# Optimization experiments

Measured on AMD Instinct MI355X. Metric: run time of the kernel, lower is better.

The kernel has to match this reference:

```python
import jax, jax.numpy as jnp
import numpy as np
from jax import lax

# channels holding diagonal entries of the embedded 4x4 bA (16:32) and bW (32:48)
_DIAG_CH = np.array([16, 21, 26, 31, 32, 37, 42, 47])
_EPS = 1e-4  # Tikhonov term for per-pixel matrix inversion stability


def _interp_matrix(out_n, in_n):
    """Dense 1D bicubic (a=-0.75) align_corners=True interpolation matrix, torch-compatible."""
    if out_n == in_n:
        return jnp.eye(out_n, dtype=jnp.float32)
    a = -0.75
    scale = (in_n - 1) / (out_n - 1)
    src = np.arange(out_n) * scale
    i0 = np.floor(src).astype(np.int64)
    W = np.zeros((out_n, in_n), np.float64)
    rows = np.arange(out_n)
    for k in range(-1, 3):
        t = np.abs(src - (i0 + k))
        w = np.where(t <= 1.0, (a + 2) * t**3 - (a + 3) * t**2 + 1.0,
                     np.where(t < 2.0, a * t**3 - 5 * a * t**2 + 8 * a * t - 4 * a, 0.0))
        np.add.at(W, (rows, np.clip(i0 + k, 0, in_n - 1)), w)  # border replication
    return jnp.asarray(W, jnp.float32)


def _conv(x, w, b):
    y = lax.conv_general_dilated(x, w, (1, 1), 'SAME',
                                 dimension_numbers=('NCHW', 'OIHW', 'NCHW'))
    return y + b[None, :, None, None]


def _leaky(x):
    return jnp.where(x >= 0, x, 0.01 * x)


def _mm_features(x):
    """compute_mm + intensity: x is (b,48,h,w) -> (b,17,h,w)."""
    b, c, h, w = x.shape
    v = jnp.moveaxis(x, 1, -1)                 # (b,h,w,48)
    F = v[..., :16].reshape(b, h, w, 4, 4)     # intensity frames
    A = v[..., 16:32].reshape(b, h, w, 4, 4)   # analyzer calib bA
    Wm = v[..., 32:48].reshape(b, h, w, 4, 4)  # generator calib bW
    eye = _EPS * jnp.eye(4, dtype=x.dtype)
    M = jnp.linalg.inv(A + eye) @ F @ jnp.linalg.inv(Wm + eye)  # M = A^-1 F W^-1
    inten = v[..., :16].mean(-1)[:, None]      # (b,1,h,w)
    m = jnp.moveaxis(M.reshape(b, h, w, 16), -1, 1)  # (b,16,h,w)
    return jnp.concatenate([inten, m], axis=1)


def _maxpool4(x):
    b, c, h, w = x.shape
    return x.reshape(b, c, h // 4, 4, w // 4, 4).max(axis=(3, 5))


def setup_inputs() -> dict:
    key = jax.random.key(0)
    ks = jax.random.split(key, 6)
    x = 0.3 * jax.random.normal(ks[0], (2, 48, 512, 512), jnp.float32)
    diag = jnp.asarray(_DIAG_CH)
    x = x.at[:, diag].add(1.0)  # well-conditioned per-pixel bA/bW ~ I + noise

    def bias48():
        return jnp.zeros((48,), jnp.float32).at[diag].set(1.0)

    iW0 = 0.05 * jax.random.normal(ks[1], (48, 48, 3, 3), jnp.float32)
    iW1 = 0.05 * jax.random.normal(ks[2], (48, 48, 3, 3), jnp.float32)
    oW0 = 0.05 * jax.random.normal(ks[3], (17, 17, 3, 3), jnp.float32)
    oW1 = 0.05 * jax.random.normal(ks[4], (17, 17, 3, 3), jnp.float32)
    return dict(x=x,
                iW0=iW0, iB0=bias48(), iW1=iW1, iB1=bias48(),
                oW0=oW0, oB0=jnp.zeros((17,), jnp.float32),
                oW1=oW1, oB1=jnp.zeros((17,), jnp.float32))


def reference(x, iW0, iB0, iW1, iB1, oW0, oB0, oW1, oB1):
    b, _, h, w = x.shape
    iparams = [(iW0, iB0), (iW1, iB1)]
    oparams = [(oW0, oB0), (oW1, oB1)]
    outs = []
    for lvl in range(2):  # fixed pyramid levels
        x = _leaky(_conv(x, *iparams[lvl]))
        m = _mm_features(x)                       # (b,17,hl,wl)
        Wh = _interp_matrix(h, m.shape[2])
        Ww = _interp_matrix(w, m.shape[3])
        m = jnp.einsum('Oh,bchw->bcOw', Wh, m)    # bicubic upsample rows
        m = jnp.einsum('Pw,bchw->bchP', Ww, m)    # bicubic upsample cols
        m = _leaky(_conv(m, *oparams[lvl]))
        outs.append(m)
        x = _maxpool4(x)
    return jnp.concatenate(outs, axis=1)          # (b,34,h,w)
```

## Files before the change

### kernel.cpp

```cpp
#include <hip/hip_runtime.h>
#include <math.h>


__device__ __forceinline__ float leakyf(float t) { return t >= 0.0f ? t : 0.01f * t; }

template<int CIN, int OCPT, int PX, int TW>
__global__ __launch_bounds__(256, 2)
void conv3x3_leaky(const float* __restrict__ in, const float* __restrict__ wgt,
                   const float* __restrict__ bias, float* __restrict__ out,
                   int H, int W, int COUT, int NG,
                   int in_bstride, int out_bstride, int out_coff)
{
    constexpr int XG     = TW / PX;
    constexpr int TH     = 256 / XG;
    constexpr int COLS   = TW + 2;
    constexpr int ROWS   = TH + 2;
    constexpr int STRIDE = (COLS + 3) & ~3;
    constexpr int TSZ    = ROWS * STRIDE;
    constexpr int ELEMS  = ROWS * COLS;
    constexpr int K      = (ELEMS + 255) / 256;
    constexpr int NV     = PX + 2;

    __shared__ float tile[2 * TSZ];
    __shared__ float wlds[CIN * OCPT * 12];
    __shared__ float blds[OCPT];

    const int tid   = threadIdx.x;
    const int tx    = tid & (XG - 1);
    const int ty    = tid / XG;
    const int g     = blockIdx.z % NG;
    const int b     = blockIdx.z / NG;
    const int obase = g * OCPT;
    const int row0  = blockIdx.y * TH;
    const int col0  = blockIdx.x * TW;
    const int HW    = H * W;

    for (int idx = tid; idx < CIN * OCPT * 9; idx += 256) {
        int c  = idx / (OCPT * 9);
        int r2 = idx - c * (OCPT * 9);
        int o  = r2 / 9;
        int k2 = r2 - o * 9;
        int og = obase + o;
        wlds[(c * OCPT + o) * 12 + k2] = (og < COUT) ? wgt[(og * CIN + c) * 9 + k2] : 0.0f;
    }
    if (tid < OCPT) {
        int og = obase + tid;
        blds[tid] = (og < COUT) ? bias[og] : 0.0f;
    }

    int goff[K], loff[K];
#pragma unroll
    for (int k = 0; k < K; ++k) {
        int idx = tid + k * 256;
        if (idx < ELEMS) {
            int r  = idx / COLS;
            int cc = idx - r * COLS;
            int gr = row0 - 1 + r;
            int gc = col0 - 1 + cc;
            bool v = (gr >= 0 && gr < H && gc >= 0 && gc < W);
            goff[k] = v ? (gr * W + gc) : -1;
            loff[k] = r * STRIDE + cc;
        } else {
            goff[k] = -1;
            loff[k] = -1;
        }
    }

    const float* inb = in + b * in_bstride;

    float sreg[K];
    {
        const float* ic = inb;
#pragma unroll
        for (int k = 0; k < K; ++k) {
            float v = 0.0f;
            if (goff[k] >= 0) v = ic[goff[k]];
            sreg[k] = v;
        }
#pragma unroll
        for (int k = 0; k < K; ++k)
            if (loff[k] >= 0) tile[loff[k]] = sreg[k];
    }
    __syncthreads();

    float acc[OCPT][PX];
#pragma unroll
    for (int o = 0; o < OCPT; ++o)
#pragma unroll
        for (int p = 0; p < PX; ++p) acc[o][p] = 0.0f;

    for (int c = 0; c < CIN; ++c) {
        if (c + 1 < CIN) {
            const float* ic = inb + (c + 1) * HW;
#pragma unroll
            for (int k = 0; k < K; ++k) {
                float v = 0.0f;
                if (goff[k] >= 0) v = ic[goff[k]];
                sreg[k] = v;
            }
        }

        {
            const float* tb = &tile[(c & 1) * TSZ];
            float v[3][NV];
#pragma unroll
            for (int rr = 0; rr < 3; ++rr) {
                const float* tp = tb + (ty + rr) * STRIDE + tx * PX;
                float4 a0 = *(const float4*)tp;
                v[rr][0] = a0.x; v[rr][1] = a0.y; v[rr][2] = a0.z; v[rr][3] = a0.w;
                if constexpr (PX == 8) {
                    float4 a1 = *(const float4*)(tp + 4);
                    float2 a2 = *(const float2*)(tp + 8);
                    v[rr][4] = a1.x; v[rr][5] = a1.y; v[rr][6] = a1.z; v[rr][7] = a1.w;
                    v[rr][8] = a2.x; v[rr][9] = a2.y;
                } else {
                    float2 a1 = *(const float2*)(tp + 4);
                    v[rr][4] = a1.x; v[rr][5] = a1.y;
                }
            }
#pragma unroll
            for (int o = 0; o < OCPT; ++o) {
                const float* wp = &wlds[(c * OCPT + o) * 12];
                float4 w0 = *(const float4*)wp;
                float4 w1 = *(const float4*)(wp + 4);
                float w8 = wp[8];
                float wk[9] = {w0.x, w0.y, w0.z, w0.w, w1.x, w1.y, w1.z, w1.w, w8};
#pragma unroll
                for (int px = 0; px < PX; ++px) {
                    float s = acc[o][px];
#pragma unroll
                    for (int kr = 0; kr < 3; ++kr)
#pragma unroll
                        for (int kc = 0; kc < 3; ++kc)
                            s = fmaf(wk[kr * 3 + kc], v[kr][px + kc], s);
                    acc[o][px] = s;
                }
            }
        }

        if (c + 1 < CIN) {
            float* tb = &tile[((c + 1) & 1) * TSZ];
#pragma unroll
            for (int k = 0; k < K; ++k)
                if (loff[k] >= 0) tb[loff[k]] = sreg[k];
            __syncthreads();
        }
    }

    const int orow = row0 + ty;
    float* outb = out + b * out_bstride;
#pragma unroll
    for (int o = 0; o < OCPT; ++o) {
        int og = obase + o;
        if (og < COUT) {
            float bv = blds[o];
            float r[PX];
#pragma unroll
            for (int p = 0; p < PX; ++p) { float t = acc[o][p] + bv; r[p] = leakyf(t); }
            float* op = outb + ((out_coff + og) * H + orow) * W + col0 + tx * PX;
#pragma unroll
            for (int q = 0; q < PX / 4; ++q)
                *(float4*)(op + 4 * q) = make_float4(r[4*q], r[4*q+1], r[4*q+2], r[4*q+3]);
        }
    }
}

__device__ __forceinline__ void inv4x4(const double* m, double* invOut)
{
    double inv[16];
    inv[0]  =  m[5]*m[10]*m[15] - m[5]*m[11]*m[14] - m[9]*m[6]*m[15] + m[9]*m[7]*m[14] + m[13]*m[6]*m[11] - m[13]*m[7]*m[10];
    inv[4]  = -m[4]*m[10]*m[15] + m[4]*m[11]*m[14] + m[8]*m[6]*m[15] - m[8]*m[7]*m[14] - m[12]*m[6]*m[11] + m[12]*m[7]*m[10];
    inv[8]  =  m[4]*m[9]*m[15]  - m[4]*m[11]*m[13] - m[8]*m[5]*m[15] + m[8]*m[7]*m[13] + m[12]*m[5]*m[11] - m[12]*m[7]*m[9];
    inv[12] = -m[4]*m[9]*m[14]  + m[4]*m[10]*m[13] + m[8]*m[5]*m[14] - m[8]*m[6]*m[13] - m[12]*m[5]*m[10] + m[12]*m[6]*m[9];
    inv[1]  = -m[1]*m[10]*m[15] + m[1]*m[11]*m[14] + m[9]*m[2]*m[15] - m[9]*m[3]*m[14] - m[13]*m[2]*m[11] + m[13]*m[3]*m[10];
    inv[5]  =  m[0]*m[10]*m[15] - m[0]*m[11]*m[14] - m[8]*m[2]*m[15] + m[8]*m[3]*m[14] + m[12]*m[2]*m[11] - m[12]*m[3]*m[10];
    inv[9]  = -m[0]*m[9]*m[15]  + m[0]*m[11]*m[13] + m[8]*m[1]*m[15] - m[8]*m[3]*m[13] - m[12]*m[1]*m[11] + m[12]*m[3]*m[9];
    inv[13] =  m[0]*m[9]*m[14]  - m[0]*m[10]*m[13] - m[8]*m[1]*m[14] + m[8]*m[2]*m[13] + m[12]*m[1]*m[10] - m[12]*m[2]*m[9];
    inv[2]  =  m[1]*m[6]*m[15]  - m[1]*m[7]*m[14]  - m[5]*m[2]*m[15] + m[5]*m[3]*m[14] + m[13]*m[2]*m[7]  - m[13]*m[3]*m[6];
    inv[6]  = -m[0]*m[6]*m[15]  + m[0]*m[7]*m[14]  + m[4]*m[2]*m[15] - m[4]*m[3]*m[14] - m[12]*m[2]*m[7]  + m[12]*m[3]*m[6];
    inv[10] =  m[0]*m[5]*m[15]  - m[0]*m[7]*m[13]  - m[4]*m[1]*m[15] + m[4]*m[3]*m[13] + m[12]*m[1]*m[7]  - m[12]*m[3]*m[5];
    inv[14] = -m[0]*m[5]*m[14]  + m[0]*m[6]*m[13]  + m[4]*m[1]*m[14] - m[4]*m[2]*m[13] - m[12]*m[1]*m[6]  + m[12]*m[2]*m[5];
    inv[3]  = -m[1]*m[6]*m[11]  + m[1]*m[7]*m[10]  + m[5]*m[2]*m[11] - m[5]*m[3]*m[10] - m[9]*m[2]*m[7]   + m[9]*m[3]*m[6];
    inv[7]  =  m[0]*m[6]*m[11]  - m[0]*m[7]*m[10]  - m[4]*m[2]*m[11] + m[4]*m[3]*m[10] + m[8]*m[2]*m[7]   - m[8]*m[3]*m[6];
    inv[11] = -m[0]*m[5]*m[11]  + m[0]*m[7]*m[9]   + m[4]*m[1]*m[11] - m[4]*m[3]*m[9]  - m[8]*m[1]*m[7]   + m[8]*m[3]*m[5];
    inv[15] =  m[0]*m[5]*m[10]  - m[0]*m[6]*m[9]   - m[4]*m[1]*m[10] + m[4]*m[2]*m[9]  + m[8]*m[1]*m[6]   - m[8]*m[2]*m[5];
    double det = m[0]*inv[0] + m[1]*inv[4] + m[2]*inv[8] + m[3]*inv[12];
    det = 1.0 / det;
#pragma unroll
    for (int i = 0; i < 16; ++i) invOut[i] = inv[i] * det;
}

__device__ __forceinline__ void matmul4(const double* A, const double* B, double* C)
{
#pragma unroll
    for (int r = 0; r < 4; ++r)
#pragma unroll
        for (int c = 0; c < 4; ++c) {
            double s = 0.0;
#pragma unroll
            for (int k = 0; k < 4; ++k) s += A[r * 4 + k] * B[k * 4 + c];
            C[r * 4 + c] = s;
        }
}

__global__ __launch_bounds__(256)
void mm_features_kernel(const float* __restrict__ y, float* __restrict__ m, int HW, int n)
{
    int p = blockIdx.x * 256 + threadIdx.x;
    if (p >= n) return;
    int b  = p / HW;
    int sp = p - b * HW;
    const float* base = y + (size_t)b * 48 * HW + sp;

    double A[16];
#pragma unroll
    for (int i = 0; i < 16; ++i) {
        double e = (i == 0 || i == 5 || i == 10 || i == 15) ? 1e-4 : 0.0;
        A[i] = (double)base[(16 + i) * HW] + e;
    }
    double iA[16];
    inv4x4(A, iA);

    double F[16];
    double s = 0.0;
#pragma unroll
    for (int i = 0; i < 16; ++i) { F[i] = (double)base[i * HW]; }
#pragma unroll
    for (int i = 0; i < 16; ++i) s += F[i];
    s *= (1.0 / 16.0);

    double T[16];
    matmul4(iA, F, T);

    double Wm[16];
#pragma unroll
    for (int i = 0; i < 16; ++i) {
        double e = (i == 0 || i == 5 || i == 10 || i == 15) ? 1e-4 : 0.0;
        Wm[i] = (double)base[(32 + i) * HW] + e;
    }
    double iW[16];
    inv4x4(Wm, iW);

    double M[16];
    matmul4(T, iW, M);

    float* ob = m + (size_t)b * 17 * HW + sp;
    ob[0] = (float)s;
#pragma unroll
    for (int i = 0; i < 16; ++i) ob[(1 + i) * HW] = (float)M[i];
}

__global__ __launch_bounds__(256)
void maxpool4_kernel(const float* __restrict__ in, float* __restrict__ out, int n)
{
    int idx = blockIdx.x * 256 + threadIdx.x;
    if (idx >= n) return;
    int ow = idx & 127;
    int oh = (idx >> 7) & 127;
    int ct = idx >> 14;
    const float* p = in + ct * 262144 + (oh * 4) * 512 + ow * 4;
    float mx = -3.4e38f;
#pragma unroll
    for (int r = 0; r < 4; ++r) {
        float4 v = *(const float4*)(p + r * 512);
        mx = fmaxf(mx, fmaxf(fmaxf(v.x, v.y), fmaxf(v.z, v.w)));
    }
    out[idx] = mx;
}

__device__ __forceinline__ double cubw(double t)
{
    const double a = -0.75;
    t = fabs(t);
    if (t <= 1.0) return ((a + 2.0) * t - (a + 3.0)) * t * t + 1.0;
    if (t < 2.0)  return (((t - 5.0) * t + 8.0) * t - 4.0) * a;
    return 0.0;
}

__global__ __launch_bounds__(256)
void bicubic_up4_kernel(const float* __restrict__ src, float* __restrict__ dst, int n)
{
    int idx = blockIdx.x * 256 + threadIdx.x;
    if (idx >= n) return;
    int P  = idx & 511;
    int O  = (idx >> 9) & 511;
    int bc = idx >> 18;
    const double scale = 127.0 / 511.0;
    double sh = O * scale, sw = P * scale;
    int i0 = (int)floor(sh), j0 = (int)floor(sw);
    double wh[4], ww[4];
#pragma unroll
    for (int k = 0; k < 4; ++k) {
        wh[k] = cubw(sh - (double)(i0 + k - 1));
        ww[k] = cubw(sw - (double)(j0 + k - 1));
    }
    const float* sp = src + bc * 16384;
    double acc = 0.0;
#pragma unroll
    for (int ki = 0; ki < 4; ++ki) {
        int ih = min(max(i0 - 1 + ki, 0), 127);
        double rs = 0.0;
#pragma unroll
        for (int kj = 0; kj < 4; ++kj) {
            int iw = min(max(j0 - 1 + kj, 0), 127);
            rs += ww[kj] * (double)sp[ih * 128 + iw];
        }
        acc += wh[ki] * rs;
    }
    dst[idx] = (float)acc;
}

extern "C" void kernel_launch(void* const* d_in, const int* in_sizes, int n_in,
                              void* d_out, int out_size, void* d_ws, size_t ws_size,
                              hipStream_t stream)
{
    const float* x   = (const float*)d_in[0];
    const float* iW0 = (const float*)d_in[1];
    const float* iB0 = (const float*)d_in[2];
    const float* iW1 = (const float*)d_in[3];
    const float* iB1 = (const float*)d_in[4];
    const float* oW0 = (const float*)d_in[5];
    const float* oB0 = (const float*)d_in[6];
    const float* oW1 = (const float*)d_in[7];
    const float* oB1 = (const float*)d_in[8];
    float* out = (float*)d_out;
    float* ws  = (float*)d_ws;

    float* y0 = ws;
    float* m0 = ws + 25165824;
    float* x1 = ws + 34078720;
    float* y1 = ws + 35651584;
    float* m1 = ws + 37224448;
    float* u  = ws;

    conv3x3_leaky<48, 8, 8, 64><<<dim3(8, 16, 12), 256, 0, stream>>>(
        x, iW0, iB0, y0, 512, 512, 48, 6, 48 * 512 * 512, 48 * 512 * 512, 0);
    mm_features_kernel<<<(2 * 512 * 512) / 256, 256, 0, stream>>>(y0, m0, 512 * 512, 2 * 512 * 512);
    conv3x3_leaky<17, 9, 8, 64><<<dim3(8, 16, 4), 256, 0, stream>>>(
        m0, oW0, oB0, out, 512, 512, 17, 2, 17 * 512 * 512, 34 * 512 * 512, 0);
    maxpool4_kernel<<<(2 * 48 * 128 * 128) / 256, 256, 0, stream>>>(y0, x1, 2 * 48 * 128 * 128);

    conv3x3_leaky<48, 4, 4, 32><<<dim3(4, 4, 24), 256, 0, stream>>>(
        x1, iW1, iB1, y1, 128, 128, 48, 12, 48 * 128 * 128, 48 * 128 * 128, 0);
    mm_features_kernel<<<(2 * 128 * 128) / 256, 256, 0, stream>>>(y1, m1, 128 * 128, 2 * 128 * 128);
    bicubic_up4_kernel<<<(2 * 17 * 512 * 512) / 256, 256, 0, stream>>>(m1, u, 2 * 17 * 512 * 512);
    conv3x3_leaky<17, 9, 8, 64><<<dim3(8, 16, 4), 256, 0, stream>>>(
        u, oW1, oB1, out, 512, 512, 17, 2, 17 * 512 * 512, 34 * 512 * 512, 17);
}
```

Measured before the change: 694.9 us.

## Use per-wavefront halo tiles to drop block barriers; compute bicubic in fp32

```diff
diff --git a/kernel.cpp b/kernel.cpp
--- a/kernel.cpp
+++ b/kernel.cpp
@@ -13,21 +13,25 @@
 {
     constexpr int XG     = TW / PX;
     constexpr int TH     = 256 / XG;
+    constexpr int RPW    = 64 / XG;
+    constexpr int NW     = 4;
     constexpr int COLS   = TW + 2;
-    constexpr int ROWS   = TH + 2;
+    constexpr int WROWS  = RPW + 2;
     constexpr int STRIDE = (COLS + 3) & ~3;
-    constexpr int TSZ    = ROWS * STRIDE;
-    constexpr int ELEMS  = ROWS * COLS;
-    constexpr int K      = (ELEMS + 255) / 256;
+    constexpr int WTSZ   = WROWS * STRIDE;
+    constexpr int WELEMS = WROWS * COLS;
+    constexpr int KW     = (WELEMS + 63) / 64;
     constexpr int NV     = PX + 2;
 
-    __shared__ float tile[2 * TSZ];
+    __shared__ float tile[NW * 2 * WTSZ];
     __shared__ float wlds[CIN * OCPT * 12];
     __shared__ float blds[OCPT];
 
     const int tid   = threadIdx.x;
     const int tx    = tid & (XG - 1);
     const int ty    = tid / XG;
+    const int lane  = tid & 63;
+    const int wv    = tid >> 6;
     const int g     = blockIdx.z % NG;
     const int b     = blockIdx.z / NG;
     const int obase = g * OCPT;
@@ -48,14 +52,14 @@
         blds[tid] = (og < COUT) ? bias[og] : 0.0f;
     }
 
-    int goff[K], loff[K];
-#pragma unroll
-    for (int k = 0; k < K; ++k) {
-        int idx = tid + k * 256;
-        if (idx < ELEMS) {
-            int r  = idx / COLS;
-            int cc = idx - r * COLS;
-            int gr = row0 - 1 + r;
+    int goff[KW], loff[KW];
+#pragma unroll
+    for (int k = 0; k < KW; ++k) {
+        int e = lane + k * 64;
+        if (e < WELEMS) {
+            int r  = e / COLS;
+            int cc = e - r * COLS;
+            int gr = row0 + wv * RPW - 1 + r;
             int gc = col0 - 1 + cc;
             bool v = (gr >= 0 && gr < H && gc >= 0 && gc < W);
             goff[k] = v ? (gr * W + gc) : -1;
@@ -67,19 +71,21 @@
     }
 
     const float* inb = in + b * in_bstride;
-
-    float sreg[K];
+    float* const wt0 = &tile[wv * 2 * WTSZ];
+    float* const wt1 = wt0 + WTSZ;
+
+    float sreg[KW];
     {
         const float* ic = inb;
 #pragma unroll
-        for (int k = 0; k < K; ++k) {
+        for (int k = 0; k < KW; ++k) {
             float v = 0.0f;
             if (goff[k] >= 0) v = ic[goff[k]];
             sreg[k] = v;
         }
 #pragma unroll
-        for (int k = 0; k < K; ++k)
-            if (loff[k] >= 0) tile[loff[k]] = sreg[k];
+        for (int k = 0; k < KW; ++k)
+            if (loff[k] >= 0) wt0[loff[k]] = sreg[k];
     }
     __syncthreads();
 
@@ -88,12 +94,14 @@
     for (int o = 0; o < OCPT; ++o)
 #pragma unroll
         for (int p = 0; p < PX; ++p) acc[o][p] = 0.0f;
+
+    const int lrow = ty & (RPW - 1);
 
     for (int c = 0; c < CIN; ++c) {
         if (c + 1 < CIN) {
             const float* ic = inb + (c + 1) * HW;
 #pragma unroll
-            for (int k = 0; k < K; ++k) {
+            for (int k = 0; k < KW; ++k) {
                 float v = 0.0f;
                 if (goff[k] >= 0) v = ic[goff[k]];
                 sreg[k] = v;
@@ -101,11 +109,11 @@
         }
 
         {
-            const float* tb = &tile[(c & 1) * TSZ];
+            const float* tb = (c & 1) ? wt1 : wt0;
             float v[3][NV];
 #pragma unroll
             for (int rr = 0; rr < 3; ++rr) {
-                const float* tp = tb + (ty + rr) * STRIDE + tx * PX;
+                const float* tp = tb + (lrow + rr) * STRIDE + tx * PX;
                 float4 a0 = *(const float4*)tp;
                 v[rr][0] = a0.x; v[rr][1] = a0.y; v[rr][2] = a0.z; v[rr][3] = a0.w;
                 if constexpr (PX == 8) {
@@ -139,11 +147,10 @@
         }
 
         if (c + 1 < CIN) {
-            float* tb = &tile[((c + 1) & 1) * TSZ];
-#pragma unroll
-            for (int k = 0; k < K; ++k)
+            float* tb = ((c + 1) & 1) ? wt1 : wt0;
+#pragma unroll
+            for (int k = 0; k < KW; ++k)
                 if (loff[k] >= 0) tb[loff[k]] = sreg[k];
-            __syncthreads();
         }
     }
 
@@ -268,13 +275,13 @@
     out[idx] = mx;
 }
 
-__device__ __forceinline__ double cubw(double t)
-{
-    const double a = -0.75;
-    t = fabs(t);
-    if (t <= 1.0) return ((a + 2.0) * t - (a + 3.0)) * t * t + 1.0;
-    if (t < 2.0)  return (((t - 5.0) * t + 8.0) * t - 4.0) * a;
-    return 0.0;
+__device__ __forceinline__ float cubwf(float t)
+{
+    const float a = -0.75f;
+    t = fabsf(t);
+    if (t <= 1.0f) return ((a + 2.0f) * t - (a + 3.0f)) * t * t + 1.0f;
+    if (t < 2.0f)  return (((t - 5.0f) * t + 8.0f) * t - 4.0f) * a;
+    return 0.0f;
 }
 
 __global__ __launch_bounds__(256)
@@ -285,29 +292,29 @@
     int P  = idx & 511;
     int O  = (idx >> 9) & 511;
     int bc = idx >> 18;
-    const double scale = 127.0 / 511.0;
-    double sh = O * scale, sw = P * scale;
-    int i0 = (int)floor(sh), j0 = (int)floor(sw);
-    double wh[4], ww[4];
+    const float scale = 127.0f / 511.0f;
+    float sh = O * scale, sw = P * scale;
+    int i0 = (int)floorf(sh), j0 = (int)floorf(sw);
+    float wh[4], ww[4];
 #pragma unroll
     for (int k = 0; k < 4; ++k) {
-        wh[k] = cubw(sh - (double)(i0 + k - 1));
-        ww[k] = cubw(sw - (double)(j0 + k - 1));
+        wh[k] = cubwf(sh - (float)(i0 + k - 1));
+        ww[k] = cubwf(sw - (float)(j0 + k - 1));
     }
     const float* sp = src + bc * 16384;
-    double acc = 0.0;
+    float acc = 0.0f;
 #pragma unroll
     for (int ki = 0; ki < 4; ++ki) {
         int ih = min(max(i0 - 1 + ki, 0), 127);
-        double rs = 0.0;
+        float rs = 0.0f;
 #pragma unroll
         for (int kj = 0; kj < 4; ++kj) {
             int iw = min(max(j0 - 1 + kj, 0), 127);
-            rs += ww[kj] * (double)sp[ih * 128 + iw];
-        }
-        acc += wh[ki] * rs;
-    }
-    dst[idx] = (float)acc;
+            rs = fmaf(ww[kj], sp[ih * 128 + iw], rs);
+        }
+        acc = fmaf(wh[ki], rs, acc);
+    }
+    dst[idx] = acc;
 }
 
 extern "C" void kernel_launch(void* const* d_in, const int* in_sizes, int n_in,
```

Result: no change. 695.8 us (+0.1%).
